# Kernel tuning notes

Measured on AMD Instinct MI355X. Metric: run time of the kernel, lower is better.

## Reference

```python
import jax, jax.numpy as jnp
import numpy as np

N = 50000      # nodes
E = 800000     # edges (avg degree 16)
D = 128        # in_dim = hidden_dim
C = 40         # num_classes
BN_EPS = 1e-5


def setup_inputs() -> dict:
    key = jax.random.key(0)
    ks = jax.random.split(key, 24)
    h = jax.random.normal(ks[0], (N, D), dtype=jnp.float32)
    edge_src = jax.random.randint(ks[1], (E,), 0, N)
    edge_dst = jax.random.randint(ks[2], (E,), 0, N)
    mask = jnp.ones((E, 1), dtype=jnp.float32)  # adj_mask2_fixed (frozen)

    def lin_w(k, fi, fo):
        return jax.random.normal(k, (fi, fo), dtype=jnp.float32) / np.sqrt(fi).astype(np.float32)

    def lin_b(k, fo):
        return jax.random.normal(k, (fo,), dtype=jnp.float32) * 0.01

    dims = [(D, D), (D, D), (D, C)]  # last GIN layer -> num_classes
    out = {"h": h, "edge_src": edge_src, "edge_dst": edge_dst, "mask": mask}
    for i, (fi, fo) in enumerate(dims):
        out[f"w{i}"] = lin_w(ks[3 + 4 * i], fi, fo)
        out[f"b{i}"] = lin_b(ks[4 + 4 * i], fo)
        out[f"g{i}"] = jnp.ones((fo,), jnp.float32) + 0.05 * jax.random.normal(ks[5 + 4 * i], (fo,), jnp.float32)
        out[f"beta{i}"] = 0.05 * jax.random.normal(ks[6 + 4 * i], (fo,), jnp.float32)
        out[f"rm{i}"] = 0.1 * jax.random.normal(jax.random.fold_in(key, 100 + i), (fo,), jnp.float32)
        out[f"rv{i}"] = jax.random.uniform(jax.random.fold_in(key, 200 + i), (fo,), jnp.float32, 0.5, 1.5)
    out["wp"] = lin_w(ks[20], D, C)
    out["bp"] = lin_b(ks[21], C)
    return out


def reference(h, edge_src, edge_dst, mask,
              w0, b0, g0, beta0, rm0, rv0,
              w1, b1, g1, beta1, rm1, rv1,
              w2, b2, g2, beta2, rm2, rv2,
              wp, bp):
    # in-degree for mean aggregation (DGL mean reducer: divide by in-degree,
    # zero for isolated nodes)
    ones_e = jnp.ones(edge_dst.shape, dtype=h.dtype)
    deg = jax.ops.segment_sum(ones_e, edge_dst, num_segments=N)
    deg_inv = jnp.where(deg > 0, 1.0 / jnp.maximum(deg, 1.0), 0.0)[:, None]

    def gin_layer(x, w, b, g, beta, rm, rv):
        msg = x[edge_src] * mask                                   # [E, d]
        agg = jax.ops.segment_sum(msg, edge_dst, num_segments=N) * deg_inv
        z = (x + agg) @ w + b                                      # (1+eps)=1, eps=0
        z = (z - rm) * jax.lax.rsqrt(rv + BN_EPS) * g + beta       # BN (eval, running stats)
        return jax.nn.relu(z)                                      # dropout: eval -> identity

    h1 = gin_layer(h, w0, b0, g0, beta0, rm0, rv0)    # [N, D]
    h2 = gin_layer(h1, w1, b1, g1, beta1, rm1, rv1)   # [N, D]  hidden_rep[-2]
    h3 = gin_layer(h2, w2, b2, g2, beta2, rm2, rv2)   # [N, C]  hidden_rep[-1]
    return ((h2 @ wp + bp) + h3) * 0.5
```

## Files before the change

kernel.cpp:

```cpp
#include <hip/hip_runtime.h>

#define N_NODES 50000
#define N_EDGES 800000
#define DIM 128
#define NCLS 40

#define NCHUNK 128
#define CE 6250
#define HALF_N 25088
#define WHALF 12544
#define SCAN_B 98
#define N_PAD 50432

typedef __bf16 bf16x8_t __attribute__((ext_vector_type(8)));
typedef unsigned short us8_t __attribute__((ext_vector_type(8)));
typedef float f32x4_t __attribute__((ext_vector_type(4)));

static __device__ __forceinline__ float b2f(unsigned short h) {
    unsigned u = ((unsigned)h) << 16;
    return __builtin_bit_cast(float, u);
}
static __device__ __forceinline__ unsigned short f2b(float f) {
    unsigned u = __builtin_bit_cast(unsigned, f);
    u += 0x7FFFu + ((u >> 16) & 1u);
    return (unsigned short)(u >> 16);
}

__global__ __launch_bounds__(256) void prep(const float* __restrict__ hsrc,
                                            unsigned short* __restrict__ hout,
                                            const float* __restrict__ w0,
                                            const float* __restrict__ w1,
                                            const float* __restrict__ w2,
                                            const float* __restrict__ wp,
                                            unsigned short* __restrict__ f0h,
                                            unsigned short* __restrict__ f0l,
                                            unsigned short* __restrict__ f1h,
                                            unsigned short* __restrict__ f1l,
                                            unsigned short* __restrict__ f2h,
                                            unsigned short* __restrict__ f2l,
                                            unsigned short* __restrict__ fph,
                                            unsigned short* __restrict__ fpl) {
    if (blockIdx.x < 3125) {
        size_t e0 = ((size_t)blockIdx.x * 256 + threadIdx.x) * 8;
        f32x4_t v0 = *(const f32x4_t*)(hsrc + e0);
        f32x4_t v1 = *(const f32x4_t*)(hsrc + e0 + 4);
        us8_t o;
        #pragma unroll
        for (int j = 0; j < 4; ++j) { o[j] = f2b(v0[j]); o[4 + j] = f2b(v1[j]); }
        *(us8_t*)(hout + e0) = o;
        return;
    }
    int t = (blockIdx.x - 3125) * 256 + threadIdx.x;
    const float* src;
    unsigned short *dh, *dl;
    int idx, ncols;
    if (t < 16384)      { src = w0; dh = f0h; dl = f0l; idx = t;         ncols = 128; }
    else if (t < 32768) { src = w1; dh = f1h; dl = f1l; idx = t - 16384; ncols = 128; }
    else if (t < 38912) { src = w2; dh = f2h; dl = f2l; idx = t - 32768; ncols = 48; }
    else if (t < 45056) { src = wp; dh = fph; dl = fpl; idx = t - 38912; ncols = 48; }
    else return;
    int k = idx / ncols, n = idx - k * ncols;
    float v;
    if (ncols == 128) v = src[k * 128 + n];
    else              v = (n < NCLS) ? src[k * NCLS + n] : 0.f;
    int nt = n >> 4, m = n & 15, kt = k >> 5, quad = (k >> 3) & 3, j = k & 7;
    int off = ((nt * 4 + kt) * 64 + quad * 16 + m) * 8 + j;
    unsigned short hi = f2b(v);
    dh[off] = hi;
    dl[off] = f2b(v - b2f(hi));
}

__global__ __launch_bounds__(256) void chunk_count(const int* __restrict__ dst,
                                                   unsigned* __restrict__ cnt) {
    __shared__ unsigned lds[WHALF];
    int c = blockIdx.x, h = blockIdx.y, tid = threadIdx.x;
    for (int w = tid; w < WHALF; w += 256) lds[w] = 0;
    __syncthreads();
    int base = c * CE;
    for (int k = tid; k < CE; k += 256) {
        int local = dst[base + k] - h * HALF_N;
        if (local >= 0 && local < HALF_N)
            atomicAdd(&lds[local >> 1], 1u << ((local & 1) * 16));
    }
    __syncthreads();
    unsigned* out = cnt + ((size_t)(h * NCHUNK + c)) * WHALF;
    for (int w = tid; w < WHALF; w += 256) out[w] = lds[w];
}

__global__ __launch_bounds__(256) void cscan(unsigned* __restrict__ cnt,
                                             unsigned* __restrict__ degp,
                                             int* __restrict__ partial) {
    __shared__ int lds[256];
    int b = blockIdx.x;
    int h = b / 49;
    int w = (b % 49) * 256 + threadIdx.x;
    unsigned acc = 0;
    for (int c = 0; c < NCHUNK; ++c) {
        size_t idx = ((size_t)(h * NCHUNK + c)) * WHALF + w;
        unsigned v = cnt[idx];
        cnt[idx] = acc;
        acc += v;
    }
    degp[h * WHALF + w] = acc;
    lds[threadIdx.x] = (int)(acc & 0xFFFFu) + (int)(acc >> 16);
    __syncthreads();
    #pragma unroll
    for (int off = 128; off > 0; off >>= 1) {
        if (threadIdx.x < off) lds[threadIdx.x] += lds[threadIdx.x + off];
        __syncthreads();
    }
    if (threadIdx.x == 0) partial[b] = lds[0];
}

__global__ __launch_bounds__(256) void scan_final(const unsigned* __restrict__ degp,
                                                  const int* __restrict__ partial,
                                                  int* __restrict__ rs,
                                                  int* __restrict__ deg,
                                                  float* __restrict__ dinv) {
    __shared__ int lds[256];
    int b = blockIdx.x;
    int h = b / 49;
    int tid = threadIdx.x;
    int w = (b % 49) * 256 + tid;
    lds[tid] = (tid < b) ? partial[tid] : 0;
    __syncthreads();
    #pragma unroll
    for (int off = 128; off > 0; off >>= 1) {
        if (tid < off) lds[tid] += lds[tid + off];
        __syncthreads();
    }
    int boff = lds[0];
    __syncthreads();
    unsigned dp = degp[h * WHALF + w];
    int lo = (int)(dp & 0xFFFFu), hi = (int)(dp >> 16);
    int s = lo + hi;
    lds[tid] = s;
    __syncthreads();
    #pragma unroll
    for (int off = 1; off < 256; off <<= 1) {
        int v = lds[tid];
        int add = (tid >= off) ? lds[tid - off] : 0;
        __syncthreads();
        lds[tid] = v + add;
        __syncthreads();
    }
    int excl = boff + lds[tid] - s;
    int n0 = h * HALF_N + 2 * w;
    rs[n0] = excl;
    rs[n0 + 1] = excl + lo;
    deg[n0] = lo;
    deg[n0 + 1] = hi;
    dinv[n0] = (lo > 0) ? (1.0f / (float)lo) : 0.0f;
    dinv[n0 + 1] = (hi > 0) ? (1.0f / (float)hi) : 0.0f;
}

__global__ __launch_bounds__(256) void fill2(const int* __restrict__ src,
                                             const int* __restrict__ dst,
                                             const float* __restrict__ mask,
                                             const unsigned* __restrict__ cnt,
                                             const int* __restrict__ rs,
                                             unsigned* __restrict__ csr) {
    __shared__ unsigned cur[WHALF];
    int c = blockIdx.x, h = blockIdx.y, tid = threadIdx.x;
    const unsigned* off = cnt + ((size_t)(h * NCHUNK + c)) * WHALF;
    for (int w = tid; w < WHALF; w += 256) cur[w] = off[w];
    __syncthreads();
    int base = c * CE;
    for (int k = tid; k < CE; k += 256) {
        int e = base + k;
        int d = dst[e];
        int local = d - h * HALF_N;
        if (local >= 0 && local < HALF_N) {
            unsigned sm = (unsigned)src[e] | ((unsigned)f2b(mask[e]) << 16);
            int sh = (local & 1) * 16;
            unsigned old = atomicAdd(&cur[local >> 1], 1u << sh);
            int rank = (int)((old >> sh) & 0xFFFFu);
            csr[rs[d] + rank] = sm;
        }
    }
}

static __device__ __forceinline__ void issue16(const unsigned short* __restrict__ xb,
                                               unsigned pk, int lane, unsigned* vv) {
    #pragma unroll
    for (int j = 0; j < 16; ++j) {
        unsigned p = (unsigned)__builtin_amdgcn_readlane((int)pk, j);
        vv[j] = *(const unsigned*)(xb + (size_t)(p & 0xFFFFu) * DIM + lane * 2);
    }
}
static __device__ __forceinline__ void accum16(unsigned pk, const unsigned* vv,
                                               float& acc0, float& acc1) {
    #pragma unroll
    for (int j = 0; j < 16; ++j) {
        unsigned p = (unsigned)__builtin_amdgcn_readlane((int)pk, j);
        float mm = b2f((unsigned short)(p >> 16));
        acc0 += mm * b2f((unsigned short)(vv[j] & 0xFFFFu));
        acc1 += mm * b2f((unsigned short)(vv[j] >> 16));
    }
}

static __device__ __forceinline__ void gather4(const unsigned short* __restrict__ xb,
                                               const float* __restrict__ xres,
                                               const int* __restrict__ rs,
                                               const int* __restrict__ deg,
                                               const float* __restrict__ dinv,
                                               const unsigned* __restrict__ csr,
                                               int nb0, int lane,
                                               float (*ldsrow)[132], int row0) {
    int rs4[4], dg4[4];
    float di4[4];
    #pragma unroll
    for (int i = 0; i < 4; ++i) {
        int n = nb0 + i;
        rs4[i] = rs[n];
        dg4[i] = deg[n];
        di4[i] = dinv[n];
    }
    unsigned pk0, pk1, pk2, pk3;
    pk0 = (lane < (dg4[0] < 16 ? dg4[0] : 16)) ? csr[rs4[0] + lane] : 0u;
    pk1 = (lane < (dg4[1] < 16 ? dg4[1] : 16)) ? csr[rs4[1] + lane] : 0u;

    unsigned vvA[16], vvB[16];
    issue16(xb, pk0, lane, vvA);

    unsigned pkq[4] = {pk0, pk1, 0u, 0u};
    #pragma unroll
    for (int i = 0; i < 4; ++i) {
        if (i == 0) pk2 = (lane < (dg4[2] < 16 ? dg4[2] : 16)) ? csr[rs4[2] + lane] : 0u;
        if (i == 1) pk3 = (lane < (dg4[3] < 16 ? dg4[3] : 16)) ? csr[rs4[3] + lane] : 0u;
        if (i == 0) pkq[2] = pk2;
        if (i == 1) pkq[3] = pk3;
        if (i < 3) issue16(xb, pkq[i + 1], lane, (i & 1) ? vvA : vvB);
        float acc0 = 0.f, acc1 = 0.f;
        accum16(pkq[i], (i & 1) ? vvB : vvA, acc0, acc1);
        for (int base = 16; base < dg4[i]; base += 16) {
            int nb = dg4[i] - base;
            if (nb > 16) nb = 16;
            unsigned pke = (lane < nb) ? csr[rs4[i] + base + lane] : 0u;
            unsigned vvE[16];
            issue16(xb, pke, lane, vvE);
            accum16(pke, vvE, acc0, acc1);
        }
        float di = di4[i];
        float2 xp = *(const float2*)(xres + (size_t)(nb0 + i) * DIM + lane * 2);
        ldsrow[row0 + i][lane * 2]     = xp.x + acc0 * di;
        ldsrow[row0 + i][lane * 2 + 1] = xp.y + acc1 * di;
    }
}

__global__ __launch_bounds__(256) void fused_layer(const unsigned short* __restrict__ xb,
                                                   const float* __restrict__ x,
                                                   const int* __restrict__ rs,
                                                   const int* __restrict__ deg,
                                                   const float* __restrict__ dinv,
                                                   const unsigned* __restrict__ csr,
                                                   const unsigned short* __restrict__ wfh,
                                                   const unsigned short* __restrict__ wfl,
                                                   const float* __restrict__ bias,
                                                   const float* __restrict__ gam,
                                                   const float* __restrict__ bet,
                                                   const float* __restrict__ rm,
                                                   const float* __restrict__ rv,
                                                   float* __restrict__ out,
                                                   unsigned short* __restrict__ outb) {
    __shared__ float lds[16][132];
    int tid = threadIdx.x;
    int wave = tid >> 6, lane = tid & 63;
    int rbase = blockIdx.x * 16;

    gather4(xb, x, rs, deg, dinv, csr, rbase + wave * 4, lane, lds, wave * 4);
    __syncthreads();

    int m = lane & 15, quad = lane >> 4;
    const float* ap = &lds[m][0];

    us8_t ah[4], al[4];
    #pragma unroll
    for (int kt = 0; kt < 4; ++kt) {
        f32x4_t p0 = *(const f32x4_t*)(ap + kt * 32 + quad * 8);
        f32x4_t p1 = *(const f32x4_t*)(ap + kt * 32 + quad * 8 + 4);
        #pragma unroll
        for (int j = 0; j < 4; ++j) {
            unsigned short h0 = f2b(p0[j]);
            unsigned short h1 = f2b(p1[j]);
            ah[kt][j] = h0;
            ah[kt][4 + j] = h1;
            al[kt][j] = f2b(p0[j] - b2f(h0));
            al[kt][4 + j] = f2b(p1[j] - b2f(h1));
        }
    }

    f32x4_t acc[2] = {};
    #pragma unroll
    for (int kt = 0; kt < 4; ++kt) {
        #pragma unroll
        for (int t = 0; t < 2; ++t) {
            int nt = wave * 2 + t;
            int boff = ((nt * 4 + kt) * 64 + lane) * 8;
            us8_t bh = *(const us8_t*)(wfh + boff);
            us8_t bl = *(const us8_t*)(wfl + boff);
            acc[t] = __builtin_amdgcn_mfma_f32_16x16x32_bf16(
                __builtin_bit_cast(bf16x8_t, ah[kt]),
                __builtin_bit_cast(bf16x8_t, bh), acc[t], 0, 0, 0);
            acc[t] = __builtin_amdgcn_mfma_f32_16x16x32_bf16(
                __builtin_bit_cast(bf16x8_t, ah[kt]),
                __builtin_bit_cast(bf16x8_t, bl), acc[t], 0, 0, 0);
            acc[t] = __builtin_amdgcn_mfma_f32_16x16x32_bf16(
                __builtin_bit_cast(bf16x8_t, al[kt]),
                __builtin_bit_cast(bf16x8_t, bh), acc[t], 0, 0, 0);
        }
    }

    #pragma unroll
    for (int t = 0; t < 2; ++t) {
        int nt = wave * 2 + t;
        int j = nt * 16 + m;
        float bj = bias[j];
        float sc = gam[j] * rsqrtf(rv[j] + 1e-5f);
        float sh = bet[j] - rm[j] * sc;
        #pragma unroll
        for (int i = 0; i < 4; ++i) {
            int r = rbase + quad * 4 + i;
            float z = fmaxf((acc[t][i] + bj) * sc + sh, 0.f);
            out[(size_t)r * DIM + j] = z;
            outb[(size_t)r * DIM + j] = f2b(z);
        }
    }
}

__global__ __launch_bounds__(256) void fused_final2(const unsigned short* __restrict__ xb,
                                                    const float* __restrict__ h2,
                                                    const int* __restrict__ rs,
                                                    const int* __restrict__ deg,
                                                    const float* __restrict__ dinv,
                                                    const unsigned* __restrict__ csr,
                                                    const unsigned short* __restrict__ f2h,
                                                    const unsigned short* __restrict__ f2l,
                                                    const unsigned short* __restrict__ fph,
                                                    const unsigned short* __restrict__ fpl,
                                                    const float* __restrict__ b2,
                                                    const float* __restrict__ g2,
                                                    const float* __restrict__ be2,
                                                    const float* __restrict__ rm2,
                                                    const float* __restrict__ rv2,
                                                    const float* __restrict__ bp,
                                                    float* __restrict__ out) {
    __shared__ float lds[16][132];
    int tid = threadIdx.x;
    int wave = tid >> 6, lane = tid & 63;
    int rbase = blockIdx.x * 16;

    gather4(xb, h2, rs, deg, dinv, csr, rbase + wave * 4, lane, lds, wave * 4);
    __syncthreads();

    if (wave == 3) return;

    int m = lane & 15, quad = lane >> 4;
    int arow = rbase + m;
    const float* ap2 = &lds[m][0];
    const float* aph = h2 + (size_t)arow * DIM;

    us8_t a2h[4], a2l[4], ahh[4], ahl[4];
    #pragma unroll
    for (int kt = 0; kt < 4; ++kt) {
        f32x4_t p0 = *(const f32x4_t*)(ap2 + kt * 32 + quad * 8);
        f32x4_t p1 = *(const f32x4_t*)(ap2 + kt * 32 + quad * 8 + 4);
        f32x4_t q0 = *(const f32x4_t*)(aph + kt * 32 + quad * 8);
        f32x4_t q1 = *(const f32x4_t*)(aph + kt * 32 + quad * 8 + 4);
        #pragma unroll
        for (int j = 0; j < 4; ++j) {
            unsigned short h0 = f2b(p0[j]), h1 = f2b(p1[j]);
            a2h[kt][j] = h0; a2h[kt][4 + j] = h1;
            a2l[kt][j] = f2b(p0[j] - b2f(h0));
            a2l[kt][4 + j] = f2b(p1[j] - b2f(h1));
            unsigned short g0 = f2b(q0[j]), g1 = f2b(q1[j]);
            ahh[kt][j] = g0; ahh[kt][4 + j] = g1;
            ahl[kt][j] = f2b(q0[j] - b2f(g0));
            ahl[kt][4 + j] = f2b(q1[j] - b2f(g1));
        }
    }

    int nt = wave;
    f32x4_t acc2 = {};
    f32x4_t accp = {};
    #pragma unroll
    for (int kt = 0; kt < 4; ++kt) {
        int boff = ((nt * 4 + kt) * 64 + lane) * 8;
        us8_t b2hv = *(const us8_t*)(f2h + boff);
        us8_t b2lv = *(const us8_t*)(f2l + boff);
        us8_t bphv = *(const us8_t*)(fph + boff);
        us8_t bplv = *(const us8_t*)(fpl + boff);
        acc2 = __builtin_amdgcn_mfma_f32_16x16x32_bf16(
            __builtin_bit_cast(bf16x8_t, a2h[kt]),
            __builtin_bit_cast(bf16x8_t, b2hv), acc2, 0, 0, 0);
        acc2 = __builtin_amdgcn_mfma_f32_16x16x32_bf16(
            __builtin_bit_cast(bf16x8_t, a2h[kt]),
            __builtin_bit_cast(bf16x8_t, b2lv), acc2, 0, 0, 0);
        acc2 = __builtin_amdgcn_mfma_f32_16x16x32_bf16(
            __builtin_bit_cast(bf16x8_t, a2l[kt]),
            __builtin_bit_cast(bf16x8_t, b2hv), acc2, 0, 0, 0);
        accp = __builtin_amdgcn_mfma_f32_16x16x32_bf16(
            __builtin_bit_cast(bf16x8_t, ahh[kt]),
            __builtin_bit_cast(bf16x8_t, bphv), accp, 0, 0, 0);
        accp = __builtin_amdgcn_mfma_f32_16x16x32_bf16(
            __builtin_bit_cast(bf16x8_t, ahh[kt]),
            __builtin_bit_cast(bf16x8_t, bplv), accp, 0, 0, 0);
        accp = __builtin_amdgcn_mfma_f32_16x16x32_bf16(
            __builtin_bit_cast(bf16x8_t, ahl[kt]),
            __builtin_bit_cast(bf16x8_t, bphv), accp, 0, 0, 0);
    }

    int j = nt * 16 + m;
    if (j < NCLS) {
        float b2j = b2[j];
        float sc = g2[j] * rsqrtf(rv2[j] + 1e-5f);
        float sh = be2[j] - rm2[j] * sc;
        float bpj = bp[j];
        #pragma unroll
        for (int i = 0; i < 4; ++i) {
            int r = rbase + quad * 4 + i;
            float z = fmaxf((acc2[i] + b2j) * sc + sh, 0.f);
            float p = accp[i] + bpj;
            out[(size_t)r * NCLS + j] = (p + z) * 0.5f;
        }
    }
}

extern "C" void kernel_launch(void* const* d_in, const int* in_sizes, int n_in,
                              void* d_out, int out_size, void* d_ws, size_t ws_size,
                              hipStream_t stream) {
    const float* h    = (const float*)d_in[0];
    const int* esrc   = (const int*)d_in[1];
    const int* edst   = (const int*)d_in[2];
    const float* mask = (const float*)d_in[3];
    const float* w0   = (const float*)d_in[4];
    const float* b0   = (const float*)d_in[5];
    const float* g0   = (const float*)d_in[6];
    const float* be0  = (const float*)d_in[7];
    const float* rm0  = (const float*)d_in[8];
    const float* rv0  = (const float*)d_in[9];
    const float* w1   = (const float*)d_in[10];
    const float* b1   = (const float*)d_in[11];
    const float* g1   = (const float*)d_in[12];
    const float* be1  = (const float*)d_in[13];
    const float* rm1  = (const float*)d_in[14];
    const float* rv1  = (const float*)d_in[15];
    const float* w2   = (const float*)d_in[16];
    const float* b2   = (const float*)d_in[17];
    const float* g2   = (const float*)d_in[18];
    const float* be2  = (const float*)d_in[19];
    const float* rm2  = (const float*)d_in[20];
    const float* rv2  = (const float*)d_in[21];
    const float* wp   = (const float*)d_in[22];
    const float* bp   = (const float*)d_in[23];

    char* ws = (char*)d_ws;
    size_t off = 0;
    auto alloc = [&](size_t bytes) {
        char* p = ws + off;
        off = (off + bytes + 255) & ~(size_t)255;
        return p;
    };
    int* rs       = (int*)alloc(N_PAD * 4);
    int* deg      = (int*)alloc(N_PAD * 4);
    float* dinv   = (float*)alloc(N_PAD * 4);
    int* partial  = (int*)alloc(128 * 4);
    unsigned* degp = (unsigned*)alloc(2 * WHALF * 4);
    unsigned* csr = (unsigned*)alloc((size_t)N_EDGES * 4);
    unsigned* cnt = (unsigned*)alloc((size_t)2 * NCHUNK * WHALF * 4);
    float* hbA    = (float*)alloc((size_t)N_NODES * DIM * 4);
    float* hbB    = (float*)alloc((size_t)N_NODES * DIM * 4);
    unsigned short* xb16  = (unsigned short*)alloc((size_t)N_NODES * DIM * 2);
    unsigned short* hbA16 = (unsigned short*)alloc((size_t)N_NODES * DIM * 2);
    unsigned short* hbB16 = (unsigned short*)alloc((size_t)N_NODES * DIM * 2);
    unsigned short* f0h = (unsigned short*)alloc(16384 * 2);
    unsigned short* f0l = (unsigned short*)alloc(16384 * 2);
    unsigned short* f1h = (unsigned short*)alloc(16384 * 2);
    unsigned short* f1l = (unsigned short*)alloc(16384 * 2);
    unsigned short* f2h = (unsigned short*)alloc(6144 * 2);
    unsigned short* f2l = (unsigned short*)alloc(6144 * 2);
    unsigned short* fph = (unsigned short*)alloc(6144 * 2);
    unsigned short* fpl = (unsigned short*)alloc(6144 * 2);

    const int GB16 = N_NODES / 16;

    prep<<<3301, 256, 0, stream>>>(h, xb16, w0, w1, w2, wp,
                                   f0h, f0l, f1h, f1l, f2h, f2l, fph, fpl);
    chunk_count<<<dim3(NCHUNK, 2), 256, 0, stream>>>(edst, cnt);
    cscan<<<SCAN_B, 256, 0, stream>>>(cnt, degp, partial);
    scan_final<<<SCAN_B, 256, 0, stream>>>(degp, partial, rs, deg, dinv);
    fill2<<<dim3(NCHUNK, 2), 256, 0, stream>>>(esrc, edst, mask, cnt, rs, csr);

    fused_layer<<<GB16, 256, 0, stream>>>(xb16, h, rs, deg, dinv, csr,
                                          f0h, f0l, b0, g0, be0, rm0, rv0, hbA, hbA16);
    fused_layer<<<GB16, 256, 0, stream>>>(hbA16, hbA, rs, deg, dinv, csr,
                                          f1h, f1l, b1, g1, be1, rm1, rv1, hbB, hbB16);
    fused_final2<<<GB16, 256, 0, stream>>>(hbB16, hbB, rs, deg, dinv, csr,
                                           f2h, f2l, fph, fpl,
                                           b2, g2, be2, rm2, rv2, bp, (float*)d_out);
}
```

Baseline: 299.9 us.

## Use one wave per node in fused GIN layers with 1024-thread blocks

Result: slower. 316.6 us (+5.6%).

```diff
diff --git a/kernel.cpp b/kernel.cpp
--- a/kernel.cpp
+++ b/kernel.cpp
@@ -180,96 +180,64 @@
     }
 }
 
-static __device__ __forceinline__ void issue16(const unsigned short* __restrict__ xb,
-                                               unsigned pk, int lane, unsigned* vv) {
-    #pragma unroll
-    for (int j = 0; j < 16; ++j) {
-        unsigned p = (unsigned)__builtin_amdgcn_readlane((int)pk, j);
-        vv[j] = *(const unsigned*)(xb + (size_t)(p & 0xFFFFu) * DIM + lane * 2);
-    }
-}
-static __device__ __forceinline__ void accum16(unsigned pk, const unsigned* vv,
-                                               float& acc0, float& acc1) {
-    #pragma unroll
-    for (int j = 0; j < 16; ++j) {
-        unsigned p = (unsigned)__builtin_amdgcn_readlane((int)pk, j);
-        float mm = b2f((unsigned short)(p >> 16));
-        acc0 += mm * b2f((unsigned short)(vv[j] & 0xFFFFu));
-        acc1 += mm * b2f((unsigned short)(vv[j] >> 16));
-    }
-}
-
-static __device__ __forceinline__ void gather4(const unsigned short* __restrict__ xb,
+static __device__ __forceinline__ void gather1(const unsigned short* __restrict__ xb,
                                                const float* __restrict__ xres,
                                                const int* __restrict__ rs,
                                                const int* __restrict__ deg,
                                                const float* __restrict__ dinv,
                                                const unsigned* __restrict__ csr,
-                                               int nb0, int lane,
-                                               float (*ldsrow)[132], int row0) {
-    int rs4[4], dg4[4];
-    float di4[4];
-    #pragma unroll
-    for (int i = 0; i < 4; ++i) {
-        int n = nb0 + i;
-        rs4[i] = rs[n];
-        dg4[i] = deg[n];
-        di4[i] = dinv[n];
-    }
-    unsigned pk0, pk1, pk2, pk3;
-    pk0 = (lane < (dg4[0] < 16 ? dg4[0] : 16)) ? csr[rs4[0] + lane] : 0u;
-    pk1 = (lane < (dg4[1] < 16 ? dg4[1] : 16)) ? csr[rs4[1] + lane] : 0u;
-
-    unsigned vvA[16], vvB[16];
-    issue16(xb, pk0, lane, vvA);
-
-    unsigned pkq[4] = {pk0, pk1, 0u, 0u};
-    #pragma unroll
-    for (int i = 0; i < 4; ++i) {
-        if (i == 0) pk2 = (lane < (dg4[2] < 16 ? dg4[2] : 16)) ? csr[rs4[2] + lane] : 0u;
-        if (i == 1) pk3 = (lane < (dg4[3] < 16 ? dg4[3] : 16)) ? csr[rs4[3] + lane] : 0u;
-        if (i == 0) pkq[2] = pk2;
-        if (i == 1) pkq[3] = pk3;
-        if (i < 3) issue16(xb, pkq[i + 1], lane, (i & 1) ? vvA : vvB);
-        float acc0 = 0.f, acc1 = 0.f;
-        accum16(pkq[i], (i & 1) ? vvB : vvA, acc0, acc1);
-        for (int base = 16; base < dg4[i]; base += 16) {
-            int nb = dg4[i] - base;
-            if (nb > 16) nb = 16;
-            unsigned pke = (lane < nb) ? csr[rs4[i] + base + lane] : 0u;
-            unsigned vvE[16];
-            issue16(xb, pke, lane, vvE);
-            accum16(pke, vvE, acc0, acc1);
-        }
-        float di = di4[i];
-        float2 xp = *(const float2*)(xres + (size_t)(nb0 + i) * DIM + lane * 2);
-        ldsrow[row0 + i][lane * 2]     = xp.x + acc0 * di;
-        ldsrow[row0 + i][lane * 2 + 1] = xp.y + acc1 * di;
-    }
-}
-
-__global__ __launch_bounds__(256) void fused_layer(const unsigned short* __restrict__ xb,
-                                                   const float* __restrict__ x,
-                                                   const int* __restrict__ rs,
-                                                   const int* __restrict__ deg,
-                                                   const float* __restrict__ dinv,
-                                                   const unsigned* __restrict__ csr,
-                                                   const unsigned short* __restrict__ wfh,
-                                                   const unsigned short* __restrict__ wfl,
-                                                   const float* __restrict__ bias,
-                                                   const float* __restrict__ gam,
-                                                   const float* __restrict__ bet,
-                                                   const float* __restrict__ rm,
-                                                   const float* __restrict__ rv,
-                                                   float* __restrict__ out,
-                                                   unsigned short* __restrict__ outb) {
+                                               int node, int lane,
+                                               float (*ldsrow)[132], int row) {
+    int start = rs[node], dg = deg[node];
+    float di = dinv[node];
+    float acc0 = 0.f, acc1 = 0.f;
+    for (int base = 0; base < dg; base += 16) {
+        int nb = dg - base;
+        if (nb > 16) nb = 16;
+        unsigned pk = (lane < nb) ? csr[start + base + lane] : 0u;
+        unsigned vv[16];
+        #pragma unroll
+        for (int j = 0; j < 16; ++j) {
+            unsigned p = (unsigned)__builtin_amdgcn_readlane((int)pk, j);
+            vv[j] = *(const unsigned*)(xb + (size_t)(p & 0xFFFFu) * DIM + lane * 2);
+        }
+        #pragma unroll
+        for (int j = 0; j < 16; ++j) {
+            unsigned p = (unsigned)__builtin_amdgcn_readlane((int)pk, j);
+            float mm = b2f((unsigned short)(p >> 16));
+            acc0 += mm * b2f((unsigned short)(vv[j] & 0xFFFFu));
+            acc1 += mm * b2f((unsigned short)(vv[j] >> 16));
+        }
+    }
+    float2 xp = *(const float2*)(xres + (size_t)node * DIM + lane * 2);
+    ldsrow[row][lane * 2]     = xp.x + acc0 * di;
+    ldsrow[row][lane * 2 + 1] = xp.y + acc1 * di;
+}
+
+__global__ __launch_bounds__(1024, 8) void fused_layer(const unsigned short* __restrict__ xb,
+                                                       const float* __restrict__ x,
+                                                       const int* __restrict__ rs,
+                                                       const int* __restrict__ deg,
+                                                       const float* __restrict__ dinv,
+                                                       const unsigned* __restrict__ csr,
+                                                       const unsigned short* __restrict__ wfh,
+                                                       const unsigned short* __restrict__ wfl,
+                                                       const float* __restrict__ bias,
+                                                       const float* __restrict__ gam,
+                                                       const float* __restrict__ bet,
+                                                       const float* __restrict__ rm,
+                                                       const float* __restrict__ rv,
+                                                       float* __restrict__ out,
+                                                       unsigned short* __restrict__ outb) {
     __shared__ float lds[16][132];
     int tid = threadIdx.x;
     int wave = tid >> 6, lane = tid & 63;
     int rbase = blockIdx.x * 16;
 
-    gather4(xb, x, rs, deg, dinv, csr, rbase + wave * 4, lane, lds, wave * 4);
-    __syncthreads();
+    gather1(xb, x, rs, deg, dinv, csr, rbase + wave, lane, lds, wave);
+    __syncthreads();
+
+    if (wave >= 8) return;
 
     int m = lane & 15, quad = lane >> 4;
     const float* ap = &lds[m][0];
@@ -290,138 +258,149 @@
         }
     }
 
-    f32x4_t acc[2] = {};
+    int nt = wave;
+    f32x4_t acc = {};
     #pragma unroll
     for (int kt = 0; kt < 4; ++kt) {
-        #pragma unroll
-        for (int t = 0; t < 2; ++t) {
-            int nt = wave * 2 + t;
-            int boff = ((nt * 4 + kt) * 64 + lane) * 8;
-            us8_t bh = *(const us8_t*)(wfh + boff);
-            us8_t bl = *(const us8_t*)(wfl + boff);
-            acc[t] = __builtin_amdgcn_mfma_f32_16x16x32_bf16(
-                __builtin_bit_cast(bf16x8_t, ah[kt]),
-                __builtin_bit_cast(bf16x8_t, bh), acc[t], 0, 0, 0);
-            acc[t] = __builtin_amdgcn_mfma_f32_16x16x32_bf16(
-                __builtin_bit_cast(bf16x8_t, ah[kt]),
-                __builtin_bit_cast(bf16x8_t, bl), acc[t], 0, 0, 0);
-            acc[t] = __builtin_amdgcn_mfma_f32_16x16x32_bf16(
-                __builtin_bit_cast(bf16x8_t, al[kt]),
-                __builtin_bit_cast(bf16x8_t, bh), acc[t], 0, 0, 0);
-        }
-    }
-
-    #pragma unroll
-    for (int t = 0; t < 2; ++t) {
-        int nt = wave * 2 + t;
-        int j = nt * 16 + m;
-        float bj = bias[j];
-        float sc = gam[j] * rsqrtf(rv[j] + 1e-5f);
-        float sh = bet[j] - rm[j] * sc;
-        #pragma unroll
-        for (int i = 0; i < 4; ++i) {
-            int r = rbase + quad * 4 + i;
-            float z = fmaxf((acc[t][i] + bj) * sc + sh, 0.f);
-            out[(size_t)r * DIM + j] = z;
-            outb[(size_t)r * DIM + j] = f2b(z);
-        }
-    }
-}
-
-__global__ __launch_bounds__(256) void fused_final2(const unsigned short* __restrict__ xb,
-                                                    const float* __restrict__ h2,
-                                                    const int* __restrict__ rs,
-                                                    const int* __restrict__ deg,
-                                                    const float* __restrict__ dinv,
-                                                    const unsigned* __restrict__ csr,
-                                                    const unsigned short* __restrict__ f2h,
-                                                    const unsigned short* __restrict__ f2l,
-                                                    const unsigned short* __restrict__ fph,
-                                                    const unsigned short* __restrict__ fpl,
-                                                    const float* __restrict__ b2,
-                                                    const float* __restrict__ g2,
-                                                    const float* __restrict__ be2,
-                                                    const float* __restrict__ rm2,
-                                                    const float* __restrict__ rv2,
-                                                    const float* __restrict__ bp,
-                                                    float* __restrict__ out) {
+        int boff = ((nt * 4 + kt) * 64 + lane) * 8;
+        us8_t bh = *(const us8_t*)(wfh + boff);
+        us8_t bl = *(const us8_t*)(wfl + boff);
+        acc = __builtin_amdgcn_mfma_f32_16x16x32_bf16(
+            __builtin_bit_cast(bf16x8_t, ah[kt]),
+            __builtin_bit_cast(bf16x8_t, bh), acc, 0, 0, 0);
+        acc = __builtin_amdgcn_mfma_f32_16x16x32_bf16(
+            __builtin_bit_cast(bf16x8_t, ah[kt]),
+            __builtin_bit_cast(bf16x8_t, bl), acc, 0, 0, 0);
+        acc = __builtin_amdgcn_mfma_f32_16x16x32_bf16(
+            __builtin_bit_cast(bf16x8_t, al[kt]),
+            __builtin_bit_cast(bf16x8_t, bh), acc, 0, 0, 0);
+    }
+
+    int j = nt * 16 + m;
+    float bj = bias[j];
+    float sc = gam[j] * rsqrtf(rv[j] + 1e-5f);
+    float sh = bet[j] - rm[j] * sc;
+    #pragma unroll
+    for (int i = 0; i < 4; ++i) {
+        int r = rbase + quad * 4 + i;
+        float z = fmaxf((acc[i] + bj) * sc + sh, 0.f);
+        out[(size_t)r * DIM + j] = z;
+        outb[(size_t)r * DIM + j] = f2b(z);
+    }
+}
+
+__global__ __launch_bounds__(1024, 8) void fused_final2(const unsigned short* __restrict__ xb,
+                                                        const float* __restrict__ h2,
+                                                        const int* __restrict__ rs,
+                                                        const int* __restrict__ deg,
+                                                        const float* __restrict__ dinv,
+                                                        const unsigned* __restrict__ csr,
+                                                        const unsigned short* __restrict__ f2h,
+                                                        const unsigned short* __restrict__ f2l,
+                                                        const unsigned short* __restrict__ fph,
+                                                        const unsigned short* __restrict__ fpl,
+                                                        const float* __restrict__ b2,
+                                                        const float* __restrict__ g2,
+                                                        const float* __restrict__ be2,
+                                                        const float* __restrict__ rm2,
+                                                        const float* __restrict__ rv2,
+                                                        const float* __restrict__ bp,
+                                                        float* __restrict__ out) {
     __shared__ float lds[16][132];
+    __shared__ float pbuf[3][16][16];
     int tid = threadIdx.x;
     int wave = tid >> 6, lane = tid & 63;
     int rbase = blockIdx.x * 16;
 
-    gather4(xb, h2, rs, deg, dinv, csr, rbase + wave * 4, lane, lds, wave * 4);
-    __syncthreads();
-
-    if (wave == 3) return;
+    gather1(xb, h2, rs, deg, dinv, csr, rbase + wave, lane, lds, wave);
+    __syncthreads();
 
     int m = lane & 15, quad = lane >> 4;
-    int arow = rbase + m;
-    const float* ap2 = &lds[m][0];
-    const float* aph = h2 + (size_t)arow * DIM;
-
-    us8_t a2h[4], a2l[4], ahh[4], ahl[4];
-    #pragma unroll
-    for (int kt = 0; kt < 4; ++kt) {
-        f32x4_t p0 = *(const f32x4_t*)(ap2 + kt * 32 + quad * 8);
-        f32x4_t p1 = *(const f32x4_t*)(ap2 + kt * 32 + quad * 8 + 4);
-        f32x4_t q0 = *(const f32x4_t*)(aph + kt * 32 + quad * 8);
-        f32x4_t q1 = *(const f32x4_t*)(aph + kt * 32 + quad * 8 + 4);
-        #pragma unroll
-        for (int j = 0; j < 4; ++j) {
-            unsigned short h0 = f2b(p0[j]), h1 = f2b(p1[j]);
-            a2h[kt][j] = h0; a2h[kt][4 + j] = h1;
-            a2l[kt][j] = f2b(p0[j] - b2f(h0));
-            a2l[kt][4 + j] = f2b(p1[j] - b2f(h1));
-            unsigned short g0 = f2b(q0[j]), g1 = f2b(q1[j]);
-            ahh[kt][j] = g0; ahh[kt][4 + j] = g1;
-            ahl[kt][j] = f2b(q0[j] - b2f(g0));
-            ahl[kt][4 + j] = f2b(q1[j] - b2f(g1));
-        }
-    }
-
-    int nt = wave;
-    f32x4_t acc2 = {};
-    f32x4_t accp = {};
-    #pragma unroll
-    for (int kt = 0; kt < 4; ++kt) {
-        int boff = ((nt * 4 + kt) * 64 + lane) * 8;
-        us8_t b2hv = *(const us8_t*)(f2h + boff);
-        us8_t b2lv = *(const us8_t*)(f2l + boff);
-        us8_t bphv = *(const us8_t*)(fph + boff);
-        us8_t bplv = *(const us8_t*)(fpl + boff);
-        acc2 = __builtin_amdgcn_mfma_f32_16x16x32_bf16(
-            __builtin_bit_cast(bf16x8_t, a2h[kt]),
-            __builtin_bit_cast(bf16x8_t, b2hv), acc2, 0, 0, 0);
-        acc2 = __builtin_amdgcn_mfma_f32_16x16x32_bf16(
-            __builtin_bit_cast(bf16x8_t, a2h[kt]),
-            __builtin_bit_cast(bf16x8_t, b2lv), acc2, 0, 0, 0);
-        acc2 = __builtin_amdgcn_mfma_f32_16x16x32_bf16(
-            __builtin_bit_cast(bf16x8_t, a2l[kt]),
-            __builtin_bit_cast(bf16x8_t, b2hv), acc2, 0, 0, 0);
-        accp = __builtin_amdgcn_mfma_f32_16x16x32_bf16(
-            __builtin_bit_cast(bf16x8_t, ahh[kt]),
-            __builtin_bit_cast(bf16x8_t, bphv), accp, 0, 0, 0);
-        accp = __builtin_amdgcn_mfma_f32_16x16x32_bf16(
-            __builtin_bit_cast(bf16x8_t, ahh[kt]),
-            __builtin_bit_cast(bf16x8_t, bplv), accp, 0, 0, 0);
-        accp = __builtin_amdgcn_mfma_f32_16x16x32_bf16(
-            __builtin_bit_cast(bf16x8_t, ahl[kt]),
-            __builtin_bit_cast(bf16x8_t, bphv), accp, 0, 0, 0);
-    }
-
-    int j = nt * 16 + m;
-    if (j < NCLS) {
-        float b2j = b2[j];
-        float sc = g2[j] * rsqrtf(rv2[j] + 1e-5f);
-        float sh = be2[j] - rm2[j] * sc;
-        float bpj = bp[j];
-        #pragma unroll
-        for (int i = 0; i < 4; ++i) {
-            int r = rbase + quad * 4 + i;
-            float z = fmaxf((acc2[i] + b2j) * sc + sh, 0.f);
-            float p = accp[i] + bpj;
-            out[(size_t)r * NCLS + j] = (p + z) * 0.5f;
+    f32x4_t myacc = {};
+
+    if (wave >= 3 && wave < 6) {
+        int nt = wave - 3;
+        const float* aph = h2 + (size_t)(rbase + m) * DIM;
+        us8_t hh[4], hl[4];
+        #pragma unroll
+        for (int kt = 0; kt < 4; ++kt) {
+            f32x4_t q0 = *(const f32x4_t*)(aph + kt * 32 + quad * 8);
+            f32x4_t q1 = *(const f32x4_t*)(aph + kt * 32 + quad * 8 + 4);
+            #pragma unroll
+            for (int j = 0; j < 4; ++j) {
+                unsigned short g0 = f2b(q0[j]), g1 = f2b(q1[j]);
+                hh[kt][j] = g0; hh[kt][4 + j] = g1;
+                hl[kt][j] = f2b(q0[j] - b2f(g0));
+                hl[kt][4 + j] = f2b(q1[j] - b2f(g1));
+            }
+        }
+        #pragma unroll
+        for (int kt = 0; kt < 4; ++kt) {
+            int boff = ((nt * 4 + kt) * 64 + lane) * 8;
+            us8_t bphv = *(const us8_t*)(fph + boff);
+            us8_t bplv = *(const us8_t*)(fpl + boff);
+            myacc = __builtin_amdgcn_mfma_f32_16x16x32_bf16(
+                __builtin_bit_cast(bf16x8_t, hh[kt]),
+                __builtin_bit_cast(bf16x8_t, bphv), myacc, 0, 0, 0);
+            myacc = __builtin_amdgcn_mfma_f32_16x16x32_bf16(
+                __builtin_bit_cast(bf16x8_t, hh[kt]),
+                __builtin_bit_cast(bf16x8_t, bplv), myacc, 0, 0, 0);
+            myacc = __builtin_amdgcn_mfma_f32_16x16x32_bf16(
+                __builtin_bit_cast(bf16x8_t, hl[kt]),
+                __builtin_bit_cast(bf16x8_t, bphv), myacc, 0, 0, 0);
+        }
+        #pragma unroll
+        for (int i = 0; i < 4; ++i)
+            pbuf[nt][quad * 4 + i][m] = myacc[i];
+    } else if (wave < 3) {
+        int nt = wave;
+        const float* ap2 = &lds[m][0];
+        us8_t a2h[4], a2l[4];
+        #pragma unroll
+        for (int kt = 0; kt < 4; ++kt) {
+            f32x4_t p0 = *(const f32x4_t*)(ap2 + kt * 32 + quad * 8);
+            f32x4_t p1 = *(const f32x4_t*)(ap2 + kt * 32 + quad * 8 + 4);
+            #pragma unroll
+            for (int j = 0; j < 4; ++j) {
+                unsigned short h0 = f2b(p0[j]), h1 = f2b(p1[j]);
+                a2h[kt][j] = h0; a2h[kt][4 + j] = h1;
+                a2l[kt][j] = f2b(p0[j] - b2f(h0));
+                a2l[kt][4 + j] = f2b(p1[j] - b2f(h1));
+            }
+        }
+        #pragma unroll
+        for (int kt = 0; kt < 4; ++kt) {
+            int boff = ((nt * 4 + kt) * 64 + lane) * 8;
+            us8_t b2hv = *(const us8_t*)(f2h + boff);
+            us8_t b2lv = *(const us8_t*)(f2l + boff);
+            myacc = __builtin_amdgcn_mfma_f32_16x16x32_bf16(
+                __builtin_bit_cast(bf16x8_t, a2h[kt]),
+                __builtin_bit_cast(bf16x8_t, b2hv), myacc, 0, 0, 0);
+            myacc = __builtin_amdgcn_mfma_f32_16x16x32_bf16(
+                __builtin_bit_cast(bf16x8_t, a2h[kt]),
+                __builtin_bit_cast(bf16x8_t, b2lv), myacc, 0, 0, 0);
+            myacc = __builtin_amdgcn_mfma_f32_16x16x32_bf16(
+                __builtin_bit_cast(bf16x8_t, a2l[kt]),
+                __builtin_bit_cast(bf16x8_t, b2hv), myacc, 0, 0, 0);
+        }
+    }
+    __syncthreads();
+
+    if (wave < 3) {
+        int nt = wave;
+        int j = nt * 16 + m;
+        if (j < NCLS) {
+            float b2j = b2[j];
+            float sc = g2[j] * rsqrtf(rv2[j] + 1e-5f);
+            float sh = be2[j] - rm2[j] * sc;
+            float bpj = bp[j];
+            #pragma unroll
+            for (int i = 0; i < 4; ++i) {
+                int r = rbase + quad * 4 + i;
+                float z = fmaxf((myacc[i] + b2j) * sc + sh, 0.f);
+                float p = pbuf[nt][quad * 4 + i][m] + bpj;
+                out[(size_t)r * NCLS + j] = (p + z) * 0.5f;
+            }
         }
     }
 }
@@ -491,11 +470,11 @@
     scan_final<<<SCAN_B, 256, 0, stream>>>(degp, partial, rs, deg, dinv);
     fill2<<<dim3(NCHUNK, 2), 256, 0, stream>>>(esrc, edst, mask, cnt, rs, csr);
 
-    fused_layer<<<GB16, 256, 0, stream>>>(xb16, h, rs, deg, dinv, csr,
-                                          f0h, f0l, b0, g0, be0, rm0, rv0, hbA, hbA16);
-    fused_layer<<<GB16, 256, 0, stream>>>(hbA16, hbA, rs, deg, dinv, csr,
-                                          f1h, f1l, b1, g1, be1, rm1, rv1, hbB, hbB16);
-    fused_final2<<<GB16, 256, 0, stream>>>(hbB16, hbB, rs, deg, dinv, csr,
-                                           f2h, f2l, fph, fpl,
-                                           b2, g2, be2, rm2, rv2, bp, (float*)d_out);
-}
+    fused_layer<<<GB16, 1024, 0, stream>>>(xb16, h, rs, deg, dinv, csr,
+                                           f0h, f0l, b0, g0, be0, rm0, rv0, hbA, hbA16);
+    fused_layer<<<GB16, 1024, 0, stream>>>(hbA16, hbA, rs, deg, dinv, csr,
+                                           f1h, f1l, b1, g1, be1, rm1, rv1, hbB, hbB16);
+    fused_final2<<<GB16, 1024, 0, stream>>>(hbB16, hbB, rs, deg, dinv, csr,
+                                            f2h, f2l, fph, fpl,
+                                            b2, g2, be2, rm2, rv2, bp, (float*)d_out);
+}
```

## Replace chunked LDS CSR build with global-atomic degree count and single-block scan

Applied to the files above, without the earlier changes.

Result: slower. 515.4 us (+71.9%).

```diff
diff --git a/kernel.cpp b/kernel.cpp
--- a/kernel.cpp
+++ b/kernel.cpp
@@ -4,12 +4,6 @@
 #define N_EDGES 800000
 #define DIM 128
 #define NCLS 40
-
-#define NCHUNK 128
-#define CE 6250
-#define HALF_N 25088
-#define WHALF 12544
-#define SCAN_B 98
 #define N_PAD 50432
 
 typedef __bf16 bf16x8_t __attribute__((ext_vector_type(8)));
@@ -25,7 +19,26 @@
     u += 0x7FFFu + ((u >> 16) & 1u);
     return (unsigned short)(u >> 16);
 }
-
+static __device__ __forceinline__ unsigned ldnt_u32(const unsigned* p) {
+    return __builtin_nontemporal_load(p);
+}
+static __device__ __forceinline__ int ldnt_i32(const int* p) {
+    return __builtin_nontemporal_load(p);
+}
+static __device__ __forceinline__ float ldnt_f32(const float* p) {
+    return __builtin_nontemporal_load(p);
+}
+static __device__ __forceinline__ float2 ldnt_f2(const float* p) {
+    unsigned long long v = __builtin_nontemporal_load((const unsigned long long*)p);
+    return __builtin_bit_cast(float2, v);
+}
+static __device__ __forceinline__ f32x4_t ldnt_f4(const float* p) {
+    return __builtin_nontemporal_load((const f32x4_t*)p);
+}
+
+#define PREP_B 3125
+#define REPACK_B 176
+#define DEG_B 200
 __global__ __launch_bounds__(256) void prep(const float* __restrict__ hsrc,
                                             unsigned short* __restrict__ hout,
                                             const float* __restrict__ w0,
@@ -39,18 +52,26 @@
                                             unsigned short* __restrict__ f2h,
                                             unsigned short* __restrict__ f2l,
                                             unsigned short* __restrict__ fph,
-                                            unsigned short* __restrict__ fpl) {
-    if (blockIdx.x < 3125) {
+                                            unsigned short* __restrict__ fpl,
+                                            const int* __restrict__ edst,
+                                            int* __restrict__ deg) {
+    if (blockIdx.x < PREP_B) {
         size_t e0 = ((size_t)blockIdx.x * 256 + threadIdx.x) * 8;
-        f32x4_t v0 = *(const f32x4_t*)(hsrc + e0);
-        f32x4_t v1 = *(const f32x4_t*)(hsrc + e0 + 4);
+        f32x4_t v0 = ldnt_f4(hsrc + e0);
+        f32x4_t v1 = ldnt_f4(hsrc + e0 + 4);
         us8_t o;
         #pragma unroll
         for (int j = 0; j < 4; ++j) { o[j] = f2b(v0[j]); o[4 + j] = f2b(v1[j]); }
         *(us8_t*)(hout + e0) = o;
         return;
     }
-    int t = (blockIdx.x - 3125) * 256 + threadIdx.x;
+    if (blockIdx.x >= PREP_B + REPACK_B) {
+        int t0 = (blockIdx.x - PREP_B - REPACK_B) * 256 + threadIdx.x;
+        for (int e = t0; e < N_EDGES; e += DEG_B * 256)
+            atomicAdd(&deg[ldnt_i32(edst + e)], 1);
+        return;
+    }
+    int t = (blockIdx.x - PREP_B) * 256 + threadIdx.x;
     const float* src;
     unsigned short *dh, *dl;
     int idx, ncols;
@@ -70,113 +91,55 @@
     dl[off] = f2b(v - b2f(hi));
 }
 
-__global__ __launch_bounds__(256) void chunk_count(const int* __restrict__ dst,
-                                                   unsigned* __restrict__ cnt) {
-    __shared__ unsigned lds[WHALF];
-    int c = blockIdx.x, h = blockIdx.y, tid = threadIdx.x;
-    for (int w = tid; w < WHALF; w += 256) lds[w] = 0;
+__global__ __launch_bounds__(1024) void scan50k(const int* __restrict__ deg,
+                                                int* __restrict__ rs,
+                                                int* __restrict__ cur,
+                                                float* __restrict__ dinv) {
+    __shared__ int lds[1024];
+    const int PER = 49;
+    int tid = threadIdx.x;
+    int s0 = tid * PER;
+    int lsum = 0;
+    for (int k = 0; k < PER; ++k) {
+        int n = s0 + k;
+        lsum += (n < N_NODES) ? deg[n] : 0;
+    }
+    lds[tid] = lsum;
     __syncthreads();
-    int base = c * CE;
-    for (int k = tid; k < CE; k += 256) {
-        int local = dst[base + k] - h * HALF_N;
-        if (local >= 0 && local < HALF_N)
-            atomicAdd(&lds[local >> 1], 1u << ((local & 1) * 16));
-    }
-    __syncthreads();
-    unsigned* out = cnt + ((size_t)(h * NCHUNK + c)) * WHALF;
-    for (int w = tid; w < WHALF; w += 256) out[w] = lds[w];
-}
-
-__global__ __launch_bounds__(256) void cscan(unsigned* __restrict__ cnt,
-                                             unsigned* __restrict__ degp,
-                                             int* __restrict__ partial) {
-    __shared__ int lds[256];
-    int b = blockIdx.x;
-    int h = b / 49;
-    int w = (b % 49) * 256 + threadIdx.x;
-    unsigned acc = 0;
-    for (int c = 0; c < NCHUNK; ++c) {
-        size_t idx = ((size_t)(h * NCHUNK + c)) * WHALF + w;
-        unsigned v = cnt[idx];
-        cnt[idx] = acc;
-        acc += v;
-    }
-    degp[h * WHALF + w] = acc;
-    lds[threadIdx.x] = (int)(acc & 0xFFFFu) + (int)(acc >> 16);
-    __syncthreads();
-    #pragma unroll
-    for (int off = 128; off > 0; off >>= 1) {
-        if (threadIdx.x < off) lds[threadIdx.x] += lds[threadIdx.x + off];
-        __syncthreads();
-    }
-    if (threadIdx.x == 0) partial[b] = lds[0];
-}
-
-__global__ __launch_bounds__(256) void scan_final(const unsigned* __restrict__ degp,
-                                                  const int* __restrict__ partial,
-                                                  int* __restrict__ rs,
-                                                  int* __restrict__ deg,
-                                                  float* __restrict__ dinv) {
-    __shared__ int lds[256];
-    int b = blockIdx.x;
-    int h = b / 49;
-    int tid = threadIdx.x;
-    int w = (b % 49) * 256 + tid;
-    lds[tid] = (tid < b) ? partial[tid] : 0;
-    __syncthreads();
-    #pragma unroll
-    for (int off = 128; off > 0; off >>= 1) {
-        if (tid < off) lds[tid] += lds[tid + off];
-        __syncthreads();
-    }
-    int boff = lds[0];
-    __syncthreads();
-    unsigned dp = degp[h * WHALF + w];
-    int lo = (int)(dp & 0xFFFFu), hi = (int)(dp >> 16);
-    int s = lo + hi;
-    lds[tid] = s;
-    __syncthreads();
-    #pragma unroll
-    for (int off = 1; off < 256; off <<= 1) {
+    #pragma unroll
+    for (int off = 1; off < 1024; off <<= 1) {
         int v = lds[tid];
         int add = (tid >= off) ? lds[tid - off] : 0;
         __syncthreads();
         lds[tid] = v + add;
         __syncthreads();
     }
-    int excl = boff + lds[tid] - s;
-    int n0 = h * HALF_N + 2 * w;
-    rs[n0] = excl;
-    rs[n0 + 1] = excl + lo;
-    deg[n0] = lo;
-    deg[n0 + 1] = hi;
-    dinv[n0] = (lo > 0) ? (1.0f / (float)lo) : 0.0f;
-    dinv[n0 + 1] = (hi > 0) ? (1.0f / (float)hi) : 0.0f;
-}
-
-__global__ __launch_bounds__(256) void fill2(const int* __restrict__ src,
-                                             const int* __restrict__ dst,
-                                             const float* __restrict__ mask,
-                                             const unsigned* __restrict__ cnt,
-                                             const int* __restrict__ rs,
-                                             unsigned* __restrict__ csr) {
-    __shared__ unsigned cur[WHALF];
-    int c = blockIdx.x, h = blockIdx.y, tid = threadIdx.x;
-    const unsigned* off = cnt + ((size_t)(h * NCHUNK + c)) * WHALF;
-    for (int w = tid; w < WHALF; w += 256) cur[w] = off[w];
-    __syncthreads();
-    int base = c * CE;
-    for (int k = tid; k < CE; k += 256) {
-        int e = base + k;
-        int d = dst[e];
-        int local = d - h * HALF_N;
-        if (local >= 0 && local < HALF_N) {
-            unsigned sm = (unsigned)src[e] | ((unsigned)f2b(mask[e]) << 16);
-            int sh = (local & 1) * 16;
-            unsigned old = atomicAdd(&cur[local >> 1], 1u << sh);
-            int rank = (int)((old >> sh) & 0xFFFFu);
-            csr[rs[d] + rank] = sm;
-        }
+    int run = lds[tid] - lsum;
+    for (int k = 0; k < PER; ++k) {
+        int n = s0 + k;
+        if (n < N_NODES) {
+            int d = deg[n];
+            rs[n] = run;
+            cur[n] = run;
+            dinv[n] = (d > 0) ? (1.0f / (float)d) : 0.0f;
+            run += d;
+        }
+    }
+}
+
+#define FILL_B 800
+__global__ __launch_bounds__(256) void fill_atomic(const int* __restrict__ esrc,
+                                                   const int* __restrict__ edst,
+                                                   const float* __restrict__ mask,
+                                                   int* __restrict__ cur,
+                                                   unsigned* __restrict__ csr) {
+    int t0 = blockIdx.x * 256 + threadIdx.x;
+    for (int e = t0; e < N_EDGES; e += FILL_B * 256) {
+        int d = ldnt_i32(edst + e);
+        int s = ldnt_i32(esrc + e);
+        float mk = ldnt_f32(mask + e);
+        int slot = atomicAdd(&cur[d], 1);
+        csr[slot] = (unsigned)s | ((unsigned)f2b(mk) << 16);
     }
 }
 
@@ -199,6 +162,7 @@
     }
 }
 
+template<bool XNT>
 static __device__ __forceinline__ void gather4(const unsigned short* __restrict__ xb,
                                                const float* __restrict__ xres,
                                                const int* __restrict__ rs,
@@ -217,8 +181,8 @@
         di4[i] = dinv[n];
     }
     unsigned pk0, pk1, pk2, pk3;
-    pk0 = (lane < (dg4[0] < 16 ? dg4[0] : 16)) ? csr[rs4[0] + lane] : 0u;
-    pk1 = (lane < (dg4[1] < 16 ? dg4[1] : 16)) ? csr[rs4[1] + lane] : 0u;
+    pk0 = (lane < (dg4[0] < 16 ? dg4[0] : 16)) ? ldnt_u32(csr + rs4[0] + lane) : 0u;
+    pk1 = (lane < (dg4[1] < 16 ? dg4[1] : 16)) ? ldnt_u32(csr + rs4[1] + lane) : 0u;
 
     unsigned vvA[16], vvB[16];
     issue16(xb, pk0, lane, vvA);
@@ -226,8 +190,8 @@
     unsigned pkq[4] = {pk0, pk1, 0u, 0u};
     #pragma unroll
     for (int i = 0; i < 4; ++i) {
-        if (i == 0) pk2 = (lane < (dg4[2] < 16 ? dg4[2] : 16)) ? csr[rs4[2] + lane] : 0u;
-        if (i == 1) pk3 = (lane < (dg4[3] < 16 ? dg4[3] : 16)) ? csr[rs4[3] + lane] : 0u;
+        if (i == 0) pk2 = (lane < (dg4[2] < 16 ? dg4[2] : 16)) ? ldnt_u32(csr + rs4[2] + lane) : 0u;
+        if (i == 1) pk3 = (lane < (dg4[3] < 16 ? dg4[3] : 16)) ? ldnt_u32(csr + rs4[3] + lane) : 0u;
         if (i == 0) pkq[2] = pk2;
         if (i == 1) pkq[3] = pk3;
         if (i < 3) issue16(xb, pkq[i + 1], lane, (i & 1) ? vvA : vvB);
@@ -236,13 +200,15 @@
         for (int base = 16; base < dg4[i]; base += 16) {
             int nb = dg4[i] - base;
             if (nb > 16) nb = 16;
-            unsigned pke = (lane < nb) ? csr[rs4[i] + base + lane] : 0u;
+            unsigned pke = (lane < nb) ? ldnt_u32(csr + rs4[i] + base + lane) : 0u;
             unsigned vvE[16];
             issue16(xb, pke, lane, vvE);
             accum16(pke, vvE, acc0, acc1);
         }
         float di = di4[i];
-        float2 xp = *(const float2*)(xres + (size_t)(nb0 + i) * DIM + lane * 2);
+        float2 xp;
+        if constexpr (XNT) xp = ldnt_f2(xres + (size_t)(nb0 + i) * DIM + lane * 2);
+        else               xp = *(const float2*)(xres + (size_t)(nb0 + i) * DIM + lane * 2);
         ldsrow[row0 + i][lane * 2]     = xp.x + acc0 * di;
         ldsrow[row0 + i][lane * 2 + 1] = xp.y + acc1 * di;
     }
@@ -268,7 +234,7 @@
     int wave = tid >> 6, lane = tid & 63;
     int rbase = blockIdx.x * 16;
 
-    gather4(xb, x, rs, deg, dinv, csr, rbase + wave * 4, lane, lds, wave * 4);
+    gather4<true>(xb, x, rs, deg, dinv, csr, rbase + wave * 4, lane, lds, wave * 4);
     __syncthreads();
 
     int m = lane & 15, quad = lane >> 4;
@@ -322,7 +288,7 @@
         for (int i = 0; i < 4; ++i) {
             int r = rbase + quad * 4 + i;
             float z = fmaxf((acc[t][i] + bj) * sc + sh, 0.f);
-            out[(size_t)r * DIM + j] = z;
+            __builtin_nontemporal_store(z, out + (size_t)r * DIM + j);
             outb[(size_t)r * DIM + j] = f2b(z);
         }
     }
@@ -350,7 +316,7 @@
     int wave = tid >> 6, lane = tid & 63;
     int rbase = blockIdx.x * 16;
 
-    gather4(xb, h2, rs, deg, dinv, csr, rbase + wave * 4, lane, lds, wave * 4);
+    gather4<false>(xb, h2, rs, deg, dinv, csr, rbase + wave * 4, lane, lds, wave * 4);
     __syncthreads();
 
     if (wave == 3) return;
@@ -421,7 +387,7 @@
             int r = rbase + quad * 4 + i;
             float z = fmaxf((acc2[i] + b2j) * sc + sh, 0.f);
             float p = accp[i] + bpj;
-            out[(size_t)r * NCLS + j] = (p + z) * 0.5f;
+            __builtin_nontemporal_store((p + z) * 0.5f, out + (size_t)r * NCLS + j);
         }
     }
 }
@@ -463,11 +429,9 @@
     };
     int* rs       = (int*)alloc(N_PAD * 4);
     int* deg      = (int*)alloc(N_PAD * 4);
+    int* cur      = (int*)alloc(N_PAD * 4);
     float* dinv   = (float*)alloc(N_PAD * 4);
-    int* partial  = (int*)alloc(128 * 4);
-    unsigned* degp = (unsigned*)alloc(2 * WHALF * 4);
     unsigned* csr = (unsigned*)alloc((size_t)N_EDGES * 4);
-    unsigned* cnt = (unsigned*)alloc((size_t)2 * NCHUNK * WHALF * 4);
     float* hbA    = (float*)alloc((size_t)N_NODES * DIM * 4);
     float* hbB    = (float*)alloc((size_t)N_NODES * DIM * 4);
     unsigned short* xb16  = (unsigned short*)alloc((size_t)N_NODES * DIM * 2);
@@ -484,12 +448,12 @@
 
     const int GB16 = N_NODES / 16;
 
-    prep<<<3301, 256, 0, stream>>>(h, xb16, w0, w1, w2, wp,
-                                   f0h, f0l, f1h, f1l, f2h, f2l, fph, fpl);
-    chunk_count<<<dim3(NCHUNK, 2), 256, 0, stream>>>(edst, cnt);
-    cscan<<<SCAN_B, 256, 0, stream>>>(cnt, degp, partial);
-    scan_final<<<SCAN_B, 256, 0, stream>>>(degp, partial, rs, deg, dinv);
-    fill2<<<dim3(NCHUNK, 2), 256, 0, stream>>>(esrc, edst, mask, cnt, rs, csr);
+    hipMemsetAsync(deg, 0, N_NODES * 4, stream);
+    prep<<<PREP_B + REPACK_B + DEG_B, 256, 0, stream>>>(
+        h, xb16, w0, w1, w2, wp,
+        f0h, f0l, f1h, f1l, f2h, f2l, fph, fpl, edst, deg);
+    scan50k<<<1, 1024, 0, stream>>>(deg, rs, cur, dinv);
+    fill_atomic<<<FILL_B, 256, 0, stream>>>(esrc, edst, mask, cur, csr);
 
     fused_layer<<<GB16, 256, 0, stream>>>(xb16, h, rs, deg, dinv, csr,
                                           f0h, f0l, b0, g0, be0, rm0, rv0, hbA, hbA16);
```
